# Kernel tuning notes

Hardware: AMD Instinct MI355X
Metric: run time of the kernel (lower is better)

## Reference

```python
import jax, jax.numpy as jnp
import numpy as np

DIM = 768
NUM_HEAD = 12
DIM_HEAD = DIM // NUM_HEAD
SCALE = DIM_HEAD ** -0.5
B, N = 4, 1024


def setup_inputs() -> dict:
    key = jax.random.key(0)
    ks = jax.random.split(key, 6)
    return {
        "x": jax.random.normal(ks[0], (B, N, DIM), jnp.float32),
        "q_weight": jax.random.normal(ks[1], (DIM, DIM), jnp.float32) * 0.02,
        "k_weight": jax.random.normal(ks[2], (DIM, DIM), jnp.float32) * 0.02,
        "v_weight": jax.random.normal(ks[3], (DIM, DIM), jnp.float32) * 0.02,
        "q_bias": jnp.zeros((DIM,), jnp.float32),
        "k_bias": jnp.zeros((DIM,), jnp.float32),
        "v_bias": jnp.zeros((DIM,), jnp.float32),
        "proj_weight": jax.random.normal(ks[4], (DIM, DIM), jnp.float32) * 0.02,
        "proj_bias": jax.random.normal(ks[5], (DIM,), jnp.float32) * 0.02,
    }


def reference(x, q_weight, k_weight, v_weight, q_bias, k_bias, v_bias,
              proj_weight, proj_bias):
    B_, N_, C = x.shape
    shortcut = x
    # pre-norm: torch .std() is unbiased (ddof=1)
    mean = jnp.mean(x, axis=-1, keepdims=True)
    std = jnp.std(x, axis=-1, keepdims=True, ddof=1)
    xn = (x - mean) / std
    # F.linear: x @ W.T + b
    q = xn @ q_weight.T + q_bias
    k = xn @ k_weight.T + k_bias
    v = xn @ v_weight.T + v_bias
    # b n (h d) -> b h n d
    q = q.reshape(B_, N_, NUM_HEAD, DIM_HEAD).transpose(0, 2, 1, 3)
    k = k.reshape(B_, N_, NUM_HEAD, DIM_HEAD).transpose(0, 2, 1, 3)
    v = v.reshape(B_, N_, NUM_HEAD, DIM_HEAD).transpose(0, 2, 1, 3)
    attn = jnp.einsum('bhqd,bhkd->bhqk', q, k * SCALE)
    attn = jax.nn.softmax(attn, axis=-1)
    out = jnp.einsum('bhqk,bhkd->bhqd', attn, v)
    out = out.transpose(0, 2, 1, 3).reshape(B_, N_, C)
    out = out @ proj_weight.T + proj_bias
    return out + shortcut
```

## Files before the change

### kernel.cpp

```cpp
#include <hip/hip_runtime.h>

typedef unsigned short ushort_t;
typedef __attribute__((ext_vector_type(8))) unsigned short ushort8;
typedef __attribute__((ext_vector_type(4))) unsigned short ushort4v;
typedef __attribute__((ext_vector_type(8))) __bf16 bf16x8;
typedef __attribute__((ext_vector_type(4))) float floatx4;

#define DIM 768
#define NHEAD 12
#define DHEAD 64
#define SEQ 1024
#define BATCH 4
#define TOKENS (BATCH * SEQ)
#define WELEM (DIM * DIM)
#define SCALE_LOG2E 0.18033688011112042f

static __device__ __forceinline__ float bf2f(ushort_t h) {
  union { unsigned int u; float f; } c;
  c.u = ((unsigned int)h) << 16;
  return c.f;
}
static __device__ __forceinline__ ushort_t f2bf(float f) {
  union { float f; unsigned int u; } c;
  c.f = f;
  unsigned int u = c.u;
  u += 0x7FFFu + ((u >> 16) & 1u);
  return (ushort_t)(u >> 16);
}
static __device__ __forceinline__ floatx4 mfma16(ushort8 a, ushort8 b, floatx4 c) {
  return __builtin_amdgcn_mfma_f32_16x16x32_bf16(
      __builtin_bit_cast(bf16x8, a), __builtin_bit_cast(bf16x8, b), c, 0, 0, 0);
}
static __device__ __forceinline__ void gload_lds16(const ushort_t* g,
                                                   ushort_t* l) {
  __builtin_amdgcn_global_load_lds(
      (const __attribute__((address_space(1))) void*)g,
      (__attribute__((address_space(3))) void*)l, 16, 0, 0);
}

__global__ __launch_bounds__(256) void cvt_kernel(
    const float* __restrict__ qw, const float* __restrict__ kw,
    const float* __restrict__ vw, const float* __restrict__ pw,
    ushort_t* __restrict__ dst) {
  const float* s = (blockIdx.y == 0) ? qw : (blockIdx.y == 1) ? kw
                  : (blockIdx.y == 2) ? vw : pw;
  ushort_t* d = dst + (size_t)blockIdx.y * WELEM;
  const int i = (blockIdx.x * 256 + threadIdx.x) * 4;
  const float4 f = *(const float4*)&s[i];
  ushort4v o;
  o[0] = f2bf(f.x); o[1] = f2bf(f.y); o[2] = f2bf(f.z); o[3] = f2bf(f.w);
  *(ushort4v*)&d[i] = o;
}

__global__ __launch_bounds__(256) void ln_kernel(const float* __restrict__ x,
                                                 ushort_t* __restrict__ xn) {
  const int wave = threadIdx.x >> 6, lane = threadIdx.x & 63;
  const int row = blockIdx.x * 4 + wave;
  const float* xr = x + (size_t)row * DIM;
  float v[12];
  float s = 0.f, s2 = 0.f;
#pragma unroll
  for (int j = 0; j < 12; ++j) {
    v[j] = xr[j * 64 + lane];
    s += v[j];
    s2 += v[j] * v[j];
  }
#pragma unroll
  for (int off = 1; off < 64; off <<= 1) {
    s += __shfl_xor(s, off);
    s2 += __shfl_xor(s2, off);
  }
  const float mean = s * (1.f / 768.f);
  const float var = (s2 - 768.f * mean * mean) * (1.f / 767.f);
  const float rstd = rsqrtf(var);
  ushort_t* xo = xn + (size_t)row * DIM;
#pragma unroll
  for (int j = 0; j < 12; ++j) xo[j * 64 + lane] = f2bf((v[j] - mean) * rstd);
}

#define BK 32
__global__ __launch_bounds__(256) void qkv_kernel(
    const ushort_t* __restrict__ xn, const ushort_t* __restrict__ wbf,
    const float* __restrict__ qb, const float* __restrict__ kb,
    const float* __restrict__ vb,
    ushort_t* __restrict__ qh, ushort_t* __restrict__ kh,
    ushort_t* __restrict__ vh) {
  __shared__ ushort_t As[128 * BK];
  __shared__ ushort_t Bs[128 * BK];
  const int tid = threadIdx.x;
  const int wave = tid >> 6, lane = tid & 63, quad = lane >> 4, l15 = lane & 15;
  const int m0 = blockIdx.x * 128;
  const int mat = blockIdx.y / 6, nb = blockIdx.y % 6;
  const int n0 = nb * 128;
  const ushort_t* W = wbf + (size_t)mat * WELEM;
  const float* bias = (mat == 0) ? qb : (mat == 1) ? kb : vb;
  ushort_t* dst = (mat == 0) ? qh : (mat == 1) ? kh : vh;
  const float oscale = (mat == 0) ? SCALE_LOG2E : 1.0f;
  const int wm = (wave >> 1) * 64, wn = (wave & 1) * 64;
  const int srow = lane >> 2, scol = (lane & 3) * 8;

  floatx4 acc[4][4];
#pragma unroll
  for (int i = 0; i < 4; ++i)
#pragma unroll
    for (int j = 0; j < 4; ++j) acc[i][j] = (floatx4){0.f, 0.f, 0.f, 0.f};

  for (int k0 = 0; k0 < DIM; k0 += BK) {
#pragma unroll
    for (int i = 0; i < 2; ++i) {
      const int c = wave * 2 + i;
      const int row = c * 16 + srow;
      gload_lds16(&xn[(size_t)(m0 + row) * DIM + k0 + scol], &As[c * 512]);
      gload_lds16(&W[(size_t)(n0 + row) * DIM + k0 + scol], &Bs[c * 512]);
    }
    __syncthreads();
    ushort8 af[4], bfr[4];
#pragma unroll
    for (int i = 0; i < 4; ++i)
      af[i] = *(const ushort8*)&As[(wm + i * 16 + l15) * BK + quad * 8];
#pragma unroll
    for (int i = 0; i < 4; ++i)
      bfr[i] = *(const ushort8*)&Bs[(wn + i * 16 + l15) * BK + quad * 8];
#pragma unroll
    for (int i = 0; i < 4; ++i)
#pragma unroll
      for (int j = 0; j < 4; ++j) acc[i][j] = mfma16(af[i], bfr[j], acc[i][j]);
    __syncthreads();
  }

#pragma unroll
  for (int i = 0; i < 4; ++i) {
#pragma unroll
    for (int j = 0; j < 4; ++j) {
      const int col = n0 + wn + j * 16 + l15;
      const float bv = bias[col];
      const int hh = col >> 6, d = col & 63;
#pragma unroll
      for (int r = 0; r < 4; ++r) {
        const int rowg = m0 + wm + i * 16 + quad * 4 + r;
        const int bb = rowg >> 10, nn = rowg & 1023;
        dst[(size_t)(((bb * NHEAD + hh) * SEQ) + nn) * DHEAD + d] =
            f2bf((acc[i][j][r] + bv) * oscale);
      }
    }
  }
}

#define KSTR 66
#define PSTR 68
__global__ __launch_bounds__(256) void attn_kernel(
    const ushort_t* __restrict__ qh, const ushort_t* __restrict__ kh,
    const ushort_t* __restrict__ vh, ushort_t* __restrict__ ao) {
  __shared__ ushort_t Ks[64 * KSTR];
  __shared__ ushort_t Vts[64 * KSTR];
  __shared__ ushort_t Ps[4][16 * PSTR];
  const int tid = threadIdx.x;
  const int wave = tid >> 6, lane = tid & 63, quad = lane >> 4, l15 = lane & 15;
  const int h = blockIdx.y, b = blockIdx.z;
  const int basekv = ((b * NHEAD + h) * SEQ) * DHEAD;
  const int q0 = blockIdx.x * 64 + wave * 16;

  ushort8 qf[2];
  {
    const ushort_t* Qr = qh + basekv + (q0 + l15) * DHEAD;
    qf[0] = *(const ushort8*)&Qr[quad * 8];
    qf[1] = *(const ushort8*)&Qr[32 + quad * 8];
  }
  ushort8 ones;
#pragma unroll
  for (int i = 0; i < 8; ++i) ones[i] = 0x3F80;

  floatx4 o[4];
#pragma unroll
  for (int t = 0; t < 4; ++t) o[t] = (floatx4){0.f, 0.f, 0.f, 0.f};
  floatx4 acc_l = (floatx4){0.f, 0.f, 0.f, 0.f};

  for (int kt = 0; kt < SEQ; kt += 64) {
#pragma unroll
    for (int p = 0; p < 2; ++p) {
      const int c = tid + p * 256;
      const int key = c >> 3, cc = c & 7;
      const ushort8 kc =
          *(const ushort8*)&kh[basekv + (kt + key) * DHEAD + cc * 8];
      *(ushort8*)&Ks[key * KSTR + cc * 8] = kc;
      const ushort8 vc =
          *(const ushort8*)&vh[basekv + (kt + key) * DHEAD + cc * 8];
      const int slot = (key & 15) * 4 + (key >> 4);
#pragma unroll
      for (int j = 0; j < 8; ++j) Vts[(cc * 8 + j) * KSTR + slot] = vc[j];
    }
    __syncthreads();

    floatx4 sacc[4];
#pragma unroll
    for (int s = 0; s < 4; ++s) sacc[s] = (floatx4){0.f, 0.f, 0.f, 0.f};
#pragma unroll
    for (int s = 0; s < 4; ++s) {
#pragma unroll
      for (int hh = 0; hh < 2; ++hh) {
        const ushort8 kf =
            *(const ushort8*)&Ks[(s * 16 + l15) * KSTR + hh * 32 + quad * 8];
        sacc[s] = mfma16(qf[hh], kf, sacc[s]);
      }
    }

#pragma unroll
    for (int r = 0; r < 4; ++r) {
      ushort4v pk;
#pragma unroll
      for (int s = 0; s < 4; ++s) pk[s] = f2bf(exp2f(sacc[s][r]));
      *(ushort4v*)&Ps[wave][(quad * 4 + r) * PSTR + l15 * 4] = pk;
    }

#pragma unroll
    for (int hh = 0; hh < 2; ++hh) {
      const ushort8 pf =
          *(const ushort8*)&Ps[wave][l15 * PSTR + hh * 32 + quad * 8];
      acc_l = mfma16(pf, ones, acc_l);
#pragma unroll
      for (int t = 0; t < 4; ++t) {
        const ushort8 vf =
            *(const ushort8*)&Vts[(t * 16 + l15) * KSTR + hh * 32 + quad * 8];
        o[t] = mfma16(pf, vf, o[t]);
      }
    }
    __syncthreads();
  }

#pragma unroll
  for (int r = 0; r < 4; ++r) {
    const float rl = 1.f / acc_l[r];
    const int qrow = q0 + quad * 4 + r;
    const int token = b * SEQ + qrow;
#pragma unroll
    for (int t = 0; t < 4; ++t)
      ao[(size_t)token * DIM + h * DHEAD + t * 16 + l15] = f2bf(o[t][r] * rl);
  }
}

__global__ __launch_bounds__(256) void proj_kernel(
    const ushort_t* __restrict__ ao, const ushort_t* __restrict__ pwb,
    const float* __restrict__ pb, const float* __restrict__ x,
    float* __restrict__ out) {
  __shared__ ushort_t As[128 * BK];
  __shared__ ushort_t Bs[128 * BK];
  const int tid = threadIdx.x;
  const int wave = tid >> 6, lane = tid & 63, quad = lane >> 4, l15 = lane & 15;
  const int m0 = blockIdx.x * 128;
  const int n0 = blockIdx.y * 128;
  const int wm = (wave >> 1) * 64, wn = (wave & 1) * 64;
  const int srow = lane >> 2, scol = (lane & 3) * 8;

  floatx4 acc[4][4];
#pragma unroll
  for (int i = 0; i < 4; ++i)
#pragma unroll
    for (int j = 0; j < 4; ++j) acc[i][j] = (floatx4){0.f, 0.f, 0.f, 0.f};

  for (int k0 = 0; k0 < DIM; k0 += BK) {
#pragma unroll
    for (int i = 0; i < 2; ++i) {
      const int c = wave * 2 + i;
      const int row = c * 16 + srow;
      gload_lds16(&ao[(size_t)(m0 + row) * DIM + k0 + scol], &As[c * 512]);
      gload_lds16(&pwb[(size_t)(n0 + row) * DIM + k0 + scol], &Bs[c * 512]);
    }
    __syncthreads();
    ushort8 af[4], bfr[4];
#pragma unroll
    for (int i = 0; i < 4; ++i)
      af[i] = *(const ushort8*)&As[(wm + i * 16 + l15) * BK + quad * 8];
#pragma unroll
    for (int i = 0; i < 4; ++i)
      bfr[i] = *(const ushort8*)&Bs[(wn + i * 16 + l15) * BK + quad * 8];
#pragma unroll
    for (int i = 0; i < 4; ++i)
#pragma unroll
      for (int j = 0; j < 4; ++j) acc[i][j] = mfma16(af[i], bfr[j], acc[i][j]);
    __syncthreads();
  }

#pragma unroll
  for (int i = 0; i < 4; ++i) {
#pragma unroll
    for (int j = 0; j < 4; ++j) {
      const int col = n0 + wn + j * 16 + l15;
      const float bv = pb[col];
#pragma unroll
      for (int r = 0; r < 4; ++r) {
        const int rowg = m0 + wm + i * 16 + quad * 4 + r;
        out[(size_t)rowg * DIM + col] =
            acc[i][j][r] + bv + x[(size_t)rowg * DIM + col];
      }
    }
  }
}

extern "C" void kernel_launch(void* const* d_in, const int* in_sizes, int n_in,
                              void* d_out, int out_size, void* d_ws,
                              size_t ws_size, hipStream_t stream) {
  const float* x  = (const float*)d_in[0];
  const float* qw = (const float*)d_in[1];
  const float* kw = (const float*)d_in[2];
  const float* vw = (const float*)d_in[3];
  const float* qb = (const float*)d_in[4];
  const float* kb = (const float*)d_in[5];
  const float* vb = (const float*)d_in[6];
  const float* pw = (const float*)d_in[7];
  const float* pb = (const float*)d_in[8];
  float* out = (float*)d_out;

  ushort_t* ws = (ushort_t*)d_ws;
  const size_t NTOK = (size_t)TOKENS * DIM;
  ushort_t* xn  = ws;
  ushort_t* qh  = ws + NTOK;
  ushort_t* kh  = ws + 2 * NTOK;
  ushort_t* vh  = ws + 3 * NTOK;
  ushort_t* wbf = ws + 4 * NTOK;
  ushort_t* ao  = xn;

  cvt_kernel<<<dim3(WELEM / 1024, 4), 256, 0, stream>>>(qw, kw, vw, pw, wbf);
  ln_kernel<<<TOKENS / 4, 256, 0, stream>>>(x, xn);
  qkv_kernel<<<dim3(32, 18), 256, 0, stream>>>(xn, wbf, qb, kb, vb, qh, kh, vh);
  attn_kernel<<<dim3(16, NHEAD, BATCH), 256, 0, stream>>>(qh, kh, vh, ao);
  proj_kernel<<<dim3(32, 6), 256, 0, stream>>>(ao, wbf + 3 * (size_t)WELEM, pb,
                                               x, out);
}
```

Baseline: 185.9 us.

## Swizzle LDS tiles, double GEMM K-tile, vectorize LN and bf16 packing

The QKV and projection GEMMs move to a 64-wide K tile with an XOR-swizzled LDS layout, which halves the barrier count and is meant to avoid bank conflicts on fragment reads. The attention kernel loads K tiles with direct global-to-LDS copies into a swizzled layout and writes V transposed as packed 32-bit pairs. LayerNorm now uses float4 loads and packed bf16 stores. bf16 conversion is simplified to round-half-up and packs two values with a byte-permute, which slightly changes rounding on ties.

```diff
diff --git a/kernel.cpp b/kernel.cpp
--- a/kernel.cpp
+++ b/kernel.cpp
@@ -1,8 +1,9 @@
 #include <hip/hip_runtime.h>
 
 typedef unsigned short ushort_t;
+typedef unsigned int uint_t;
 typedef __attribute__((ext_vector_type(8))) unsigned short ushort8;
-typedef __attribute__((ext_vector_type(4))) unsigned short ushort4v;
+typedef __attribute__((ext_vector_type(2))) unsigned int uint2v;
 typedef __attribute__((ext_vector_type(8))) __bf16 bf16x8;
 typedef __attribute__((ext_vector_type(4))) float floatx4;
 
@@ -15,17 +16,19 @@
 #define WELEM (DIM * DIM)
 #define SCALE_LOG2E 0.18033688011112042f
 
-static __device__ __forceinline__ float bf2f(ushort_t h) {
-  union { unsigned int u; float f; } c;
-  c.u = ((unsigned int)h) << 16;
-  return c.f;
+static __device__ __forceinline__ uint_t fbits(float f) {
+  union { float f; uint_t u; } c; c.f = f; return c.u;
 }
 static __device__ __forceinline__ ushort_t f2bf(float f) {
-  union { float f; unsigned int u; } c;
-  c.f = f;
-  unsigned int u = c.u;
-  u += 0x7FFFu + ((u >> 16) & 1u);
-  return (ushort_t)(u >> 16);
+  return (ushort_t)((fbits(f) + 0x8000u) >> 16);
+}
+static __device__ __forceinline__ uint_t pack_bf2(float lo, float hi) {
+  const uint_t a = fbits(lo) + 0x8000u, b = fbits(hi) + 0x8000u;
+#if __has_builtin(__builtin_amdgcn_perm)
+  return __builtin_amdgcn_perm(b, a, 0x07060302u);
+#else
+  return (a >> 16) | (b & 0xFFFF0000u);
+#endif
 }
 static __device__ __forceinline__ floatx4 mfma16(ushort8 a, ushort8 b, floatx4 c) {
   return __builtin_amdgcn_mfma_f32_16x16x32_bf16(
@@ -47,23 +50,24 @@
   ushort_t* d = dst + (size_t)blockIdx.y * WELEM;
   const int i = (blockIdx.x * 256 + threadIdx.x) * 4;
   const float4 f = *(const float4*)&s[i];
-  ushort4v o;
-  o[0] = f2bf(f.x); o[1] = f2bf(f.y); o[2] = f2bf(f.z); o[3] = f2bf(f.w);
-  *(ushort4v*)&d[i] = o;
+  uint2v o;
+  o[0] = pack_bf2(f.x, f.y);
+  o[1] = pack_bf2(f.z, f.w);
+  *(uint2v*)&d[i] = o;
 }
 
 __global__ __launch_bounds__(256) void ln_kernel(const float* __restrict__ x,
                                                  ushort_t* __restrict__ xn) {
   const int wave = threadIdx.x >> 6, lane = threadIdx.x & 63;
   const int row = blockIdx.x * 4 + wave;
-  const float* xr = x + (size_t)row * DIM;
-  float v[12];
+  const float4* xr = (const float4*)(x + (size_t)row * DIM);
+  float4 v[3];
   float s = 0.f, s2 = 0.f;
 #pragma unroll
-  for (int j = 0; j < 12; ++j) {
+  for (int j = 0; j < 3; ++j) {
     v[j] = xr[j * 64 + lane];
-    s += v[j];
-    s2 += v[j] * v[j];
+    s += v[j].x + v[j].y + v[j].z + v[j].w;
+    s2 += v[j].x * v[j].x + v[j].y * v[j].y + v[j].z * v[j].z + v[j].w * v[j].w;
   }
 #pragma unroll
   for (int off = 1; off < 64; off <<= 1) {
@@ -75,10 +79,15 @@
   const float rstd = rsqrtf(var);
   ushort_t* xo = xn + (size_t)row * DIM;
 #pragma unroll
-  for (int j = 0; j < 12; ++j) xo[j * 64 + lane] = f2bf((v[j] - mean) * rstd);
-}
-
-#define BK 32
+  for (int j = 0; j < 3; ++j) {
+    uint2v o;
+    o[0] = pack_bf2((v[j].x - mean) * rstd, (v[j].y - mean) * rstd);
+    o[1] = pack_bf2((v[j].z - mean) * rstd, (v[j].w - mean) * rstd);
+    *(uint2v*)&xo[(j * 64 + lane) * 4] = o;
+  }
+}
+
+#define BK 64
 __global__ __launch_bounds__(256) void qkv_kernel(
     const ushort_t* __restrict__ xn, const ushort_t* __restrict__ wbf,
     const float* __restrict__ qb, const float* __restrict__ kb,
@@ -97,7 +106,9 @@
   ushort_t* dst = (mat == 0) ? qh : (mat == 1) ? kh : vh;
   const float oscale = (mat == 0) ? SCALE_LOG2E : 1.0f;
   const int wm = (wave >> 1) * 64, wn = (wave & 1) * 64;
-  const int srow = lane >> 2, scol = (lane & 3) * 8;
+  const int srow = lane >> 3;
+  const int schunk = (lane & 7) ^ srow;
+  const int l7 = l15 & 7;
 
   floatx4 acc[4][4];
 #pragma unroll
@@ -107,24 +118,29 @@
 
   for (int k0 = 0; k0 < DIM; k0 += BK) {
 #pragma unroll
-    for (int i = 0; i < 2; ++i) {
-      const int c = wave * 2 + i;
-      const int row = c * 16 + srow;
-      gload_lds16(&xn[(size_t)(m0 + row) * DIM + k0 + scol], &As[c * 512]);
-      gload_lds16(&W[(size_t)(n0 + row) * DIM + k0 + scol], &Bs[c * 512]);
-    }
-    __syncthreads();
-    ushort8 af[4], bfr[4];
+    for (int i = 0; i < 4; ++i) {
+      const int c = wave * 4 + i;
+      const int row = c * 8 + srow;
+      gload_lds16(&xn[(size_t)(m0 + row) * DIM + k0 + schunk * 8], &As[c * 512]);
+      gload_lds16(&W[(size_t)(n0 + row) * DIM + k0 + schunk * 8], &Bs[c * 512]);
+    }
+    __syncthreads();
+    ushort8 af[4][2], bfr[4][2];
 #pragma unroll
     for (int i = 0; i < 4; ++i)
-      af[i] = *(const ushort8*)&As[(wm + i * 16 + l15) * BK + quad * 8];
-#pragma unroll
-    for (int i = 0; i < 4; ++i)
-      bfr[i] = *(const ushort8*)&Bs[(wn + i * 16 + l15) * BK + quad * 8];
-#pragma unroll
-    for (int i = 0; i < 4; ++i)
-#pragma unroll
-      for (int j = 0; j < 4; ++j) acc[i][j] = mfma16(af[i], bfr[j], acc[i][j]);
+#pragma unroll
+      for (int kh = 0; kh < 2; ++kh) {
+        const int ch = ((kh * 4 + quad) ^ l7) * 8;
+        af[i][kh] = *(const ushort8*)&As[(wm + i * 16 + l15) * BK + ch];
+        bfr[i][kh] = *(const ushort8*)&Bs[(wn + i * 16 + l15) * BK + ch];
+      }
+#pragma unroll
+    for (int kh = 0; kh < 2; ++kh)
+#pragma unroll
+      for (int i = 0; i < 4; ++i)
+#pragma unroll
+        for (int j = 0; j < 4; ++j)
+          acc[i][j] = mfma16(af[i][kh], bfr[j][kh], acc[i][j]);
     __syncthreads();
   }
 
@@ -151,7 +167,7 @@
 __global__ __launch_bounds__(256) void attn_kernel(
     const ushort_t* __restrict__ qh, const ushort_t* __restrict__ kh,
     const ushort_t* __restrict__ vh, ushort_t* __restrict__ ao) {
-  __shared__ ushort_t Ks[64 * KSTR];
+  __shared__ ushort_t Ks[64 * 64];
   __shared__ ushort_t Vts[64 * KSTR];
   __shared__ ushort_t Ps[4][16 * PSTR];
   const int tid = threadIdx.x;
@@ -159,6 +175,7 @@
   const int h = blockIdx.y, b = blockIdx.z;
   const int basekv = ((b * NHEAD + h) * SEQ) * DHEAD;
   const int q0 = blockIdx.x * 64 + wave * 16;
+  const int l7 = l15 & 7;
 
   ushort8 qf[2];
   {
@@ -175,19 +192,27 @@
   for (int t = 0; t < 4; ++t) o[t] = (floatx4){0.f, 0.f, 0.f, 0.f};
   floatx4 acc_l = (floatx4){0.f, 0.f, 0.f, 0.f};
 
+  const int ksrow = lane >> 3, kschunk = (lane & 7) ^ ksrow;
+  const int vp = tid >> 3, vcc = tid & 7;
+  const int vl = vp & 15, vs0 = (vp >> 4) << 1;
+  const int kA = vs0 * 16 + vl;
+
   for (int kt = 0; kt < SEQ; kt += 64) {
 #pragma unroll
-    for (int p = 0; p < 2; ++p) {
-      const int c = tid + p * 256;
-      const int key = c >> 3, cc = c & 7;
-      const ushort8 kc =
-          *(const ushort8*)&kh[basekv + (kt + key) * DHEAD + cc * 8];
-      *(ushort8*)&Ks[key * KSTR + cc * 8] = kc;
-      const ushort8 vc =
-          *(const ushort8*)&vh[basekv + (kt + key) * DHEAD + cc * 8];
-      const int slot = (key & 15) * 4 + (key >> 4);
-#pragma unroll
-      for (int j = 0; j < 8; ++j) Vts[(cc * 8 + j) * KSTR + slot] = vc[j];
+    for (int i = 0; i < 2; ++i) {
+      const int c = wave * 2 + i;
+      gload_lds16(&kh[basekv + (kt + c * 8 + ksrow) * DHEAD + kschunk * 8],
+                  &Ks[c * 512]);
+    }
+    {
+      const ushort8 vA =
+          *(const ushort8*)&vh[basekv + (kt + kA) * DHEAD + vcc * 8];
+      const ushort8 vB =
+          *(const ushort8*)&vh[basekv + (kt + kA + 16) * DHEAD + vcc * 8];
+#pragma unroll
+      for (int j = 0; j < 8; ++j)
+        *(uint_t*)&Vts[(vcc * 8 + j) * KSTR + vl * 4 + vs0] =
+            (uint_t)vA[j] | ((uint_t)vB[j] << 16);
     }
     __syncthreads();
 
@@ -198,18 +223,18 @@
     for (int s = 0; s < 4; ++s) {
 #pragma unroll
       for (int hh = 0; hh < 2; ++hh) {
-        const ushort8 kf =
-            *(const ushort8*)&Ks[(s * 16 + l15) * KSTR + hh * 32 + quad * 8];
+        const ushort8 kf = *(const ushort8*)&Ks[(s * 16 + l15) * 64 +
+                                                (((hh * 4 + quad) ^ l7) * 8)];
         sacc[s] = mfma16(qf[hh], kf, sacc[s]);
       }
     }
 
 #pragma unroll
     for (int r = 0; r < 4; ++r) {
-      ushort4v pk;
-#pragma unroll
-      for (int s = 0; s < 4; ++s) pk[s] = f2bf(exp2f(sacc[s][r]));
-      *(ushort4v*)&Ps[wave][(quad * 4 + r) * PSTR + l15 * 4] = pk;
+      uint2v pk;
+      pk[0] = pack_bf2(exp2f(sacc[0][r]), exp2f(sacc[1][r]));
+      pk[1] = pack_bf2(exp2f(sacc[2][r]), exp2f(sacc[3][r]));
+      *(uint2v*)&Ps[wave][(quad * 4 + r) * PSTR + l15 * 4] = pk;
     }
 
 #pragma unroll
@@ -249,7 +274,9 @@
   const int m0 = blockIdx.x * 128;
   const int n0 = blockIdx.y * 128;
   const int wm = (wave >> 1) * 64, wn = (wave & 1) * 64;
-  const int srow = lane >> 2, scol = (lane & 3) * 8;
+  const int srow = lane >> 3;
+  const int schunk = (lane & 7) ^ srow;
+  const int l7 = l15 & 7;
 
   floatx4 acc[4][4];
 #pragma unroll
@@ -259,24 +286,29 @@
 
   for (int k0 = 0; k0 < DIM; k0 += BK) {
 #pragma unroll
-    for (int i = 0; i < 2; ++i) {
-      const int c = wave * 2 + i;
-      const int row = c * 16 + srow;
-      gload_lds16(&ao[(size_t)(m0 + row) * DIM + k0 + scol], &As[c * 512]);
-      gload_lds16(&pwb[(size_t)(n0 + row) * DIM + k0 + scol], &Bs[c * 512]);
-    }
-    __syncthreads();
-    ushort8 af[4], bfr[4];
+    for (int i = 0; i < 4; ++i) {
+      const int c = wave * 4 + i;
+      const int row = c * 8 + srow;
+      gload_lds16(&ao[(size_t)(m0 + row) * DIM + k0 + schunk * 8], &As[c * 512]);
+      gload_lds16(&pwb[(size_t)(n0 + row) * DIM + k0 + schunk * 8], &Bs[c * 512]);
+    }
+    __syncthreads();
+    ushort8 af[4][2], bfr[4][2];
 #pragma unroll
     for (int i = 0; i < 4; ++i)
-      af[i] = *(const ushort8*)&As[(wm + i * 16 + l15) * BK + quad * 8];
-#pragma unroll
-    for (int i = 0; i < 4; ++i)
-      bfr[i] = *(const ushort8*)&Bs[(wn + i * 16 + l15) * BK + quad * 8];
-#pragma unroll
-    for (int i = 0; i < 4; ++i)
-#pragma unroll
-      for (int j = 0; j < 4; ++j) acc[i][j] = mfma16(af[i], bfr[j], acc[i][j]);
+#pragma unroll
+      for (int kh = 0; kh < 2; ++kh) {
+        const int ch = ((kh * 4 + quad) ^ l7) * 8;
+        af[i][kh] = *(const ushort8*)&As[(wm + i * 16 + l15) * BK + ch];
+        bfr[i][kh] = *(const ushort8*)&Bs[(wn + i * 16 + l15) * BK + ch];
+      }
+#pragma unroll
+    for (int kh = 0; kh < 2; ++kh)
+#pragma unroll
+      for (int i = 0; i < 4; ++i)
+#pragma unroll
+        for (int j = 0; j < 4; ++j)
+          acc[i][j] = mfma16(af[i][kh], bfr[j][kh], acc[i][j]);
     __syncthreads();
   }
 
```

Result: faster. 170.6 us (-8.2%).
